# Performance work log

Hardware: AMD Instinct MI355X
Metric: run time of the kernel (lower is better)

## Reference

```python
import jax, jax.numpy as jnp
import numpy as np

EMBED_DIM = 768
NUM_HEADS = 12
HEAD_DIM = EMBED_DIM // NUM_HEADS
SCALE = HEAD_DIM ** -0.5


def setup_inputs() -> dict:
    key = jax.random.key(0)
    k_x, k_wqkv, k_bqkv, k_wfc, k_bfc = jax.random.split(key, 5)
    B, S, D = 32, 577, EMBED_DIM
    x = jax.random.normal(k_x, (B, S, D), dtype=jnp.float32)
    # torch Linear default init ~ U(-1/sqrt(fan_in), 1/sqrt(fan_in)); scale suffices
    lim = 1.0 / np.sqrt(D)
    w_qkv = jax.random.uniform(k_wqkv, (D, 3 * D), jnp.float32, -lim, lim)
    b_qkv = jax.random.uniform(k_bqkv, (3 * D,), jnp.float32, -lim, lim)
    w_fc = jax.random.uniform(k_wfc, (D, D), jnp.float32, -lim, lim)
    b_fc = jax.random.uniform(k_bfc, (D,), jnp.float32, -lim, lim)
    return {"x": x, "w_qkv": w_qkv, "b_qkv": b_qkv, "w_fc": w_fc, "b_fc": b_fc}


def reference(x, w_qkv, b_qkv, w_fc, b_fc):
    B, S, D = x.shape
    H, Dh = NUM_HEADS, HEAD_DIM
    qkv = x @ w_qkv + b_qkv                      # [B,S,3D]
    qkv = qkv.reshape(B, S, 3, H, Dh)
    q, k, v = jnp.moveaxis(qkv, 2, 0)            # each [B,S,H,Dh]
    # scores: [B,H,S,S]
    attn = jnp.einsum('bqhd,bkhd->bhqk', q, k) * SCALE
    attn = jax.nn.softmax(attn, axis=-1)
    out = jnp.einsum('bhqk,bkhd->bqhd', attn, v).reshape(B, S, D)
    # dropout in eval mode -> identity
    return out @ w_fc + b_fc
```

## Files before the change

### kernel.cpp

```cpp
#include <hip/hip_runtime.h>
#include <hip/hip_bf16.h>
#include <stdint.h>

typedef __attribute__((ext_vector_type(8))) short short8;
typedef __attribute__((ext_vector_type(4))) float f32x4;

typedef __attribute__((address_space(3))) uint8_t lds_u8;
typedef __attribute__((address_space(1))) uint8_t glb_u8;

__device__ __forceinline__ void load_lds_16(const void* g, void* l) {
    __builtin_amdgcn_global_load_lds((glb_u8*)g, (lds_u8*)l, 16, 0, 0);
}

__device__ __forceinline__ unsigned short f2b(float f) {
    __hip_bfloat16 h = __float2bfloat16(f);
    return __builtin_bit_cast(unsigned short, h);
}
__device__ __forceinline__ ushort2 f2b2(float a, float b) {
    __hip_bfloat162 h = __float22bfloat162_rn(float2{a, b});
    ushort2 r;
    __builtin_memcpy(&r, &h, sizeof(r));
    return r;
}
__device__ __forceinline__ float b2f(unsigned short u) {
    unsigned int x = ((unsigned int)u) << 16;
    return __builtin_bit_cast(float, x);
}

constexpr int Bz = 32, Ss = 577, Dd = 768, Hh = 12;
constexpr int Mm = Bz * Ss;
constexpr int QKV_N = 3 * Dd;
constexpr float SCALE_L2E = 0.125f * 1.4426950408889634f;

__global__ void cast_f32_bf16(const float* __restrict__ src,
                              unsigned short* __restrict__ dst, int n4) {
    int i = blockIdx.x * blockDim.x + threadIdx.x;
    if (i >= n4) return;
    float4 v = ((const float4*)src)[i];
    ushort4 o;
    o.x = f2b(v.x); o.y = f2b(v.y); o.z = f2b(v.z); o.w = f2b(v.w);
    ((ushort4*)dst)[i] = o;
}

__global__ void transpose_cast(const float* __restrict__ src,
                               unsigned short* __restrict__ dst, int R, int C) {
    __shared__ unsigned short tile[32][33];
    int c0 = blockIdx.x * 32, r0 = blockIdx.y * 32;
    int tx = threadIdx.x, ty = threadIdx.y;
#pragma unroll
    for (int i = 0; i < 4; ++i)
        tile[ty + i * 8][tx] = f2b(src[(size_t)(r0 + ty + i * 8) * C + c0 + tx]);
    __syncthreads();
#pragma unroll
    for (int i = 0; i < 4; ++i) {
        int rr = ty + i * 8;
        dst[(size_t)(c0 + rr) * R + r0 + tx] = tile[tx][rr];
    }
}

template <int N_, bool OUT_BF16>
__global__ __launch_bounds__(512, 2)
void gemm256(const unsigned short* __restrict__ A,
             const unsigned short* __restrict__ Bt,
             const float* __restrict__ bias,
             void* __restrict__ Cout) {
    constexpr int K = 768;
    constexpr int KB = 24;
    constexpr int NX = N_ / 256;
    constexpr int NY = (Mm + 255) / 256;
    constexpr int NWG = NX * NY;
    constexpr int QC = NWG >> 3, RC = NWG & 7;
    extern __shared__ __align__(16) uint8_t smem[];

    const int tid = threadIdx.x;
    const int wave = tid >> 6, lane = tid & 63;
    const int quad = lane >> 4, lc = lane & 15;
    const int wm = wave >> 2, wn = wave & 3;

    const int orig = blockIdx.y * NX + blockIdx.x;
    const int xcd = orig & 7, lid = orig >> 3;
    const int wgid = (xcd < RC ? xcd * (QC + 1) : RC * (QC + 1) + (xcd - RC) * QC) + lid;
    const int tm = (wgid / NX) * 256;
    const int tn = (wgid % NX) * 256;

    const int lrw = wave * 8 + (lane >> 3);
    const unsigned short* apS[2];
    const unsigned short* bpS[2];
#pragma unroll
    for (int s = 0; s < 2; ++s) {
        const int lr = s * 64 + lrw;
        const int chun = (lane & 7) ^ (lr & 7);
        const int trow = lr * 2 + (chun >> 2);
        int ar = tm + trow; if (ar >= Mm) ar = Mm - 1;
        apS[s] = A + (size_t)ar * K + (chun & 3) * 8;
        const int br = tn + trow;
        bpS[s] = Bt + (size_t)br * K + (chun & 3) * 8;
    }

    auto stage = [&](int kb, int buf) {
        uint8_t* d = smem + buf * 32768 + wave * 1024;
        const int ko = kb * 32;
        load_lds_16(apS[0] + ko, d);
        load_lds_16(apS[1] + ko, d + 8192);
        load_lds_16(bpS[0] + ko, d + 16384);
        load_lds_16(bpS[1] + ko, d + 24576);
    };

    const int slotS = (((lane & 1) << 2) + quad) ^ ((lc >> 1) & 7);
    const int aoff = (wm * 64 + (lc >> 1)) * 128 + slotS * 16;
    const int boff = 16384 + (wn * 32 + (lc >> 1)) * 128 + slotS * 16;

    short8 af[8], bf[4];
    auto readfr = [&](int buf) {
        const uint8_t* p = smem + buf * 32768;
#pragma unroll
        for (int m = 0; m < 8; ++m) af[m] = *(const short8*)(p + aoff + m * 1024);
#pragma unroll
        for (int n = 0; n < 4; ++n) bf[n] = *(const short8*)(p + boff + n * 1024);
    };

    f32x4 acc[8][4] = {};
    auto mfmas = [&]() {
        __builtin_amdgcn_s_setprio(1);
#pragma unroll
        for (int m = 0; m < 8; ++m)
#pragma unroll
            for (int n = 0; n < 4; ++n)
                acc[m][n] = __builtin_amdgcn_mfma_f32_16x16x32_bf16(af[m], bf[n], acc[m][n], 0, 0, 0);
        __builtin_amdgcn_s_setprio(0);
    };

    stage(0, 0);
    stage(1, 1);
    asm volatile("s_waitcnt vmcnt(4)" ::: "memory");
    __builtin_amdgcn_s_barrier();

#pragma unroll 1
    for (int t3 = 0; t3 < 7; ++t3) {
        const int T = t3 * 3;
#pragma unroll
        for (int u = 0; u < 3; ++u) {
            const int rb = u;
            const int sb = (u + 2) % 3;
            stage(T + u + 2, sb);
            readfr(rb);
            mfmas();
            asm volatile("s_waitcnt vmcnt(4)" ::: "memory");
            __builtin_amdgcn_s_barrier();
        }
    }
    stage(23, 2);
    readfr(0);
    mfmas();
    asm volatile("s_waitcnt vmcnt(4)" ::: "memory");
    __builtin_amdgcn_s_barrier();
    readfr(1);
    mfmas();
    asm volatile("s_waitcnt vmcnt(0)" ::: "memory");
    __builtin_amdgcn_s_barrier();
    readfr(2);
    mfmas();
    __builtin_amdgcn_s_barrier();

    float bv[4];
#pragma unroll
    for (int j = 0; j < 4; ++j) bv[j] = bias[tn + wn * 64 + j * 16 + lc];

    float* ep = (float*)smem + wave * (16 * 68);
    const int erow = lane >> 2, ec = (lane & 3) * 16;
#pragma unroll
    for (int ia = 0; ia < 8; ++ia) {
#pragma unroll
        for (int j = 0; j < 4; ++j)
#pragma unroll
            for (int r = 0; r < 4; ++r)
                ep[(quad * 4 + r) * 68 + j * 16 + lc] = acc[ia][j][r] + bv[j];
        __threadfence_block();
        int grow = tm + wm * 128 + ia * 16 + erow;
        if (grow < Mm) {
            float4 c0 = *(float4*)&ep[erow * 68 + ec + 0];
            float4 c1 = *(float4*)&ep[erow * 68 + ec + 4];
            float4 c2 = *(float4*)&ep[erow * 68 + ec + 8];
            float4 c3 = *(float4*)&ep[erow * 68 + ec + 12];
            int gcol = tn + wn * 64 + ec;
            if constexpr (OUT_BF16) {
                unsigned short o[16];
                *(ushort2*)&o[0]  = f2b2(c0.x, c0.y);
                *(ushort2*)&o[2]  = f2b2(c0.z, c0.w);
                *(ushort2*)&o[4]  = f2b2(c1.x, c1.y);
                *(ushort2*)&o[6]  = f2b2(c1.z, c1.w);
                *(ushort2*)&o[8]  = f2b2(c2.x, c2.y);
                *(ushort2*)&o[10] = f2b2(c2.z, c2.w);
                *(ushort2*)&o[12] = f2b2(c3.x, c3.y);
                *(ushort2*)&o[14] = f2b2(c3.z, c3.w);
                unsigned short* op = (unsigned short*)Cout + (size_t)grow * N_ + gcol;
                *(short8*)(op + 0) = *(short8*)&o[0];
                *(short8*)(op + 8) = *(short8*)&o[8];
            } else {
                float* op = (float*)Cout + (size_t)grow * N_ + gcol;
                *(float4*)(op + 0)  = c0;
                *(float4*)(op + 4)  = c1;
                *(float4*)(op + 8)  = c2;
                *(float4*)(op + 12) = c3;
            }
        }
        __threadfence_block();
    }
}

__device__ __forceinline__ void attn_tile(
    const unsigned short* __restrict__ Ktile,
    const unsigned short* __restrict__ Vtb,
    unsigned short* __restrict__ Pqw,
    const short8& qf0, const short8& qf1,
    int quad, int lc,
    f32x4 (&oacc)[4], f32x4& lacc) {

    const int sw = lc & 7;
    f32x4 sfr[4];
    __builtin_amdgcn_s_setprio(1);
#pragma unroll
    for (int f = 0; f < 4; ++f) {
        const unsigned short* kr = Ktile + (f * 16 + lc) * 64;
        short8 k0 = *(const short8*)(kr + (quad ^ sw) * 8);
        short8 k1 = *(const short8*)(kr + ((quad ^ 4) ^ sw) * 8);
        f32x4 z = {};
        z = __builtin_amdgcn_mfma_f32_16x16x32_bf16(k0, qf0, z, 0, 0, 0);
        z = __builtin_amdgcn_mfma_f32_16x16x32_bf16(k1, qf1, z, 0, 0, 0);
        sfr[f] = z;
    }
    __builtin_amdgcn_s_setprio(0);

#pragma unroll
    for (int f = 0; f < 4; ++f) {
        float p[4];
#pragma unroll
        for (int r = 0; r < 4; ++r)
            p[r] = __builtin_amdgcn_exp2f(sfr[f][r] * SCALE_L2E);
        ushort2 lo = f2b2(p[0], p[1]), hi = f2b2(p[2], p[3]);
        ushort4 pk = {lo.x, lo.y, hi.x, hi.y};
        *(ushort4*)&Pqw[lc * 72 + f * 16 + quad * 4] = pk;
    }

    __threadfence_block();

    short8 pf0 = *(const short8*)&Pqw[lc * 72 + quad * 8];
    short8 pf1 = *(const short8*)&Pqw[lc * 72 + 32 + quad * 8];
    __builtin_amdgcn_s_setprio(1);
#pragma unroll
    for (int g = 0; g < 4; ++g) {
        short8 vf0 = *(const short8*)&Vtb[(g * 16 + lc) * 80 + quad * 8];
        short8 vf1 = *(const short8*)&Vtb[(g * 16 + lc) * 80 + 32 + quad * 8];
        oacc[g] = __builtin_amdgcn_mfma_f32_16x16x32_bf16(vf0, pf0, oacc[g], 0, 0, 0);
        oacc[g] = __builtin_amdgcn_mfma_f32_16x16x32_bf16(vf1, pf1, oacc[g], 0, 0, 0);
    }
    short8 vo0 = *(const short8*)&Vtb[(64 + lc) * 80 + quad * 8];
    short8 vo1 = *(const short8*)&Vtb[(64 + lc) * 80 + 32 + quad * 8];
    lacc = __builtin_amdgcn_mfma_f32_16x16x32_bf16(vo0, pf0, lacc, 0, 0, 0);
    lacc = __builtin_amdgcn_mfma_f32_16x16x32_bf16(vo1, pf1, lacc, 0, 0, 0);
    __builtin_amdgcn_s_setprio(0);
}

__global__ __launch_bounds__(512)
void attn_kernel(const unsigned short* __restrict__ qkv,
                 unsigned short* __restrict__ outb) {
    __shared__ unsigned short Kt[2][64 * 64];
    __shared__ unsigned short Vt[2][80 * 80];
    __shared__ unsigned short Pq[8][16 * 72];

    const int tid = threadIdx.x;
    const int wave = tid >> 6, lane = tid & 63;
    const int quad = lane >> 4, lc = lane & 15;

    const int orig = (blockIdx.z * gridDim.y + blockIdx.y) * gridDim.x + blockIdx.x;
    const int wgid = (orig & 7) * 240 + (orig >> 3);
    const int qt = wgid % 5;
    const int h  = (wgid / 5) % Hh;
    const int b  = wgid / (5 * Hh);

    const unsigned short* qkvK = qkv + (size_t)b * Ss * QKV_N + h * 64 + 768;
    const unsigned short* qkvV = qkvK + 768;

    const int krow = lane >> 3;
    const int gch = (lane & 7) ^ krow;

    const int qbase = qt * 128 + wave * 16;
    int qrow = qbase + lc; if (qrow > Ss - 1) qrow = Ss - 1;
    const unsigned short* qp = qkv + (size_t)(b * Ss + qrow) * QKV_N + h * 64;
    short8 qf0 = *(const short8*)(qp + quad * 8);
    short8 qf1 = *(const short8*)(qp + 32 + quad * 8);

    unsigned short* Pqw = Pq[wave];

    auto stage_K = [&](int tile, int buf) {
        int key = tile * 64 + wave * 8 + krow;
        const unsigned short* gp = qkvK + (size_t)key * QKV_N + gch * 8;
        load_lds_16(gp, (void*)&Kt[buf][wave * 512]);
    };
    auto load_V = [&](int tile) -> short8 {
        int key = tile * 64 + lane;
        return *(const short8*)(qkvV + (size_t)key * QKV_N + wave * 8);
    };
    auto write_V = [&](short8 v, int buf) {
#pragma unroll
        for (int j = 0; j < 8; ++j)
            Vt[buf][(wave * 8 + j) * 80 + lane] = (unsigned short)v[j];
    };

    if (tid < 80) {
        Vt[0][64 * 80 + tid] = 0x3F80;
        Vt[1][64 * 80 + tid] = 0x3F80;
    }

    f32x4 oacc[4] = {};
    f32x4 lacc = {};

    stage_K(0, 0);
    write_V(load_V(0), 0);
    __syncthreads();

    for (int kb = 0; kb < 8; ++kb) {
        const int buf = kb & 1;
        stage_K(kb + 1, buf ^ 1);
        short8 vreg = load_V(kb + 1);
        attn_tile(Kt[buf], Vt[buf], Pqw, qf0, qf1, quad, lc, oacc, lacc);
        write_V(vreg, buf ^ 1);
        __syncthreads();
    }
    attn_tile(Kt[0], Vt[0], Pqw, qf0, qf1, quad, lc, oacc, lacc);

    float ptail;
    {
        const unsigned short* k576 = qkvK + (size_t)576 * QKV_N;
        short8 kk0 = *(const short8*)(k576 + quad * 8);
        short8 kk1 = *(const short8*)(k576 + 32 + quad * 8);
        float part = 0.f;
#pragma unroll
        for (int j = 0; j < 8; ++j)
            part += b2f((unsigned short)qf0[j]) * b2f((unsigned short)kk0[j])
                  + b2f((unsigned short)qf1[j]) * b2f((unsigned short)kk1[j]);
        part += __shfl_xor(part, 16, 64);
        part += __shfl_xor(part, 32, 64);
        ptail = __builtin_amdgcn_exp2f(part * SCALE_L2E);
        const unsigned short* v576 = qkvV + (size_t)576 * QKV_N;
#pragma unroll
        for (int g = 0; g < 4; ++g) {
            ushort4 vv = *(const ushort4*)(v576 + g * 16 + quad * 4);
            oacc[g][0] += ptail * b2f(vv.x);
            oacc[g][1] += ptail * b2f(vv.y);
            oacc[g][2] += ptail * b2f(vv.z);
            oacc[g][3] += ptail * b2f(vv.w);
        }
    }

    float lq = __shfl(lacc[0], lc, 64) + ptail;
    float inv = 1.f / lq;
#pragma unroll
    for (int g = 0; g < 4; ++g) {
        ushort2 lo = f2b2(oacc[g][0] * inv, oacc[g][1] * inv);
        ushort2 hi = f2b2(oacc[g][2] * inv, oacc[g][3] * inv);
        ushort4 ob = {lo.x, lo.y, hi.x, hi.y};
        *(ushort4*)&Pqw[lc * 72 + g * 16 + quad * 4] = ob;
    }
    __threadfence_block();
#pragma unroll
    for (int p = 0; p < 2; ++p) {
        int lr = p * 8 + (lane >> 3), ch = lane & 7;
        int q = qbase + lr;
        if (q <= Ss - 1) {
            short8 vv = *(const short8*)&Pqw[lr * 72 + ch * 8];
            *(short8*)(outb + (size_t)(b * Ss + q) * Dd + h * 64 + ch * 8) = vv;
        }
    }
}

extern "C" void kernel_launch(void* const* d_in, const int* in_sizes, int n_in,
                              void* d_out, int out_size, void* d_ws, size_t ws_size,
                              hipStream_t stream) {
    const float* x     = (const float*)d_in[0];
    const float* w_qkv = (const float*)d_in[1];
    const float* b_qkv = (const float*)d_in[2];
    const float* w_fc  = (const float*)d_in[3];
    const float* b_fc  = (const float*)d_in[4];

    uint8_t* ws = (uint8_t*)d_ws;
    unsigned short* xb    = (unsigned short*)(ws + 0);
    unsigned short* wqkvT = (unsigned short*)(ws + 28360704);
    unsigned short* wfcT  = (unsigned short*)(ws + 31899648);
    unsigned short* qkv   = (unsigned short*)(ws + 33079296);
    unsigned short* attn  = (unsigned short*)(ws + 118161408);

    static bool lds_init = false;
    if (!lds_init) {
        hipFuncSetAttribute((const void*)gemm256<QKV_N, true>,
                            hipFuncAttributeMaxDynamicSharedMemorySize, 98304);
        hipFuncSetAttribute((const void*)gemm256<Dd, false>,
                            hipFuncAttributeMaxDynamicSharedMemorySize, 98304);
        lds_init = true;
    }

    int n4 = (Mm * Dd) / 4;
    cast_f32_bf16<<<(n4 + 255) / 256, 256, 0, stream>>>(x, xb, n4);
    transpose_cast<<<dim3(QKV_N / 32, Dd / 32), dim3(32, 8), 0, stream>>>(w_qkv, wqkvT, Dd, QKV_N);
    transpose_cast<<<dim3(Dd / 32, Dd / 32), dim3(32, 8), 0, stream>>>(w_fc, wfcT, Dd, Dd);

    gemm256<QKV_N, true><<<dim3(QKV_N / 256, (Mm + 255) / 256), 512, 98304, stream>>>(xb, wqkvT, b_qkv, qkv);

    attn_kernel<<<dim3(5, Hh, Bz), 512, 0, stream>>>(qkv, attn);

    gemm256<Dd, false><<<dim3(Dd / 256, (Mm + 255) / 256), 512, 98304, stream>>>(attn, wfcT, b_fc, d_out);
}
```

Baseline: 312.3 us.

## Give each attention wave 32 query rows to reuse K/V fragments; fuse prep kernels

```diff
diff --git a/kernel.cpp b/kernel.cpp
--- a/kernel.cpp
+++ b/kernel.cpp
@@ -32,21 +32,36 @@
 constexpr int QKV_N = 3 * Dd;
 constexpr float SCALE_L2E = 0.125f * 1.4426950408889634f;
 
-__global__ void cast_f32_bf16(const float* __restrict__ src,
-                              unsigned short* __restrict__ dst, int n4) {
-    int i = blockIdx.x * blockDim.x + threadIdx.x;
-    if (i >= n4) return;
-    float4 v = ((const float4*)src)[i];
-    ushort4 o;
-    o.x = f2b(v.x); o.y = f2b(v.y); o.z = f2b(v.z); o.w = f2b(v.w);
-    ((ushort4*)dst)[i] = o;
-}
-
-__global__ void transpose_cast(const float* __restrict__ src,
-                               unsigned short* __restrict__ dst, int R, int C) {
+__global__ void prep_fused(const float* __restrict__ x, unsigned short* __restrict__ xb,
+                           const float* __restrict__ w_qkv, unsigned short* __restrict__ wqkvT,
+                           const float* __restrict__ w_fc, unsigned short* __restrict__ wfcT) {
+    constexpr int N4 = Mm * Dd / 4;
+    constexpr int NC = N4 / 256;
+    constexpr int NT1 = (QKV_N / 32) * (Dd / 32);
     __shared__ unsigned short tile[32][33];
-    int c0 = blockIdx.x * 32, r0 = blockIdx.y * 32;
-    int tx = threadIdx.x, ty = threadIdx.y;
+
+    const int bid = blockIdx.x;
+    const int tid = threadIdx.x;
+    if (bid < NC) {
+        int i = bid * 256 + tid;
+        float4 v = ((const float4*)x)[i];
+        ushort4 o;
+        o.x = f2b(v.x); o.y = f2b(v.y); o.z = f2b(v.z); o.w = f2b(v.w);
+        ((ushort4*)xb)[i] = o;
+        return;
+    }
+    const float* src; unsigned short* dst; int R, C, bx, by;
+    if (bid < NC + NT1) {
+        int b2 = bid - NC;
+        src = w_qkv; dst = wqkvT; R = Dd; C = QKV_N;
+        bx = b2 % (QKV_N / 32); by = b2 / (QKV_N / 32);
+    } else {
+        int b2 = bid - NC - NT1;
+        src = w_fc; dst = wfcT; R = Dd; C = Dd;
+        bx = b2 % (Dd / 32); by = b2 / (Dd / 32);
+    }
+    int c0 = bx * 32, r0 = by * 32;
+    int tx = tid & 31, ty = tid >> 5;
 #pragma unroll
     for (int i = 0; i < 4; ++i)
         tile[ty + i * 8][tx] = f2b(src[(size_t)(r0 + ty + i * 8) * C + c0 + tx]);
@@ -65,7 +80,6 @@
              const float* __restrict__ bias,
              void* __restrict__ Cout) {
     constexpr int K = 768;
-    constexpr int KB = 24;
     constexpr int NX = N_ / 256;
     constexpr int NY = (Mm + 255) / 256;
     constexpr int NWG = NX * NY;
@@ -140,10 +154,9 @@
         const int T = t3 * 3;
 #pragma unroll
         for (int u = 0; u < 3; ++u) {
-            const int rb = u;
             const int sb = (u + 2) % 3;
             stage(T + u + 2, sb);
-            readfr(rb);
+            readfr(u);
             mfmas();
             asm volatile("s_waitcnt vmcnt(4)" ::: "memory");
             __builtin_amdgcn_s_barrier();
@@ -208,65 +221,12 @@
     }
 }
 
-__device__ __forceinline__ void attn_tile(
-    const unsigned short* __restrict__ Ktile,
-    const unsigned short* __restrict__ Vtb,
-    unsigned short* __restrict__ Pqw,
-    const short8& qf0, const short8& qf1,
-    int quad, int lc,
-    f32x4 (&oacc)[4], f32x4& lacc) {
-
-    const int sw = lc & 7;
-    f32x4 sfr[4];
-    __builtin_amdgcn_s_setprio(1);
-#pragma unroll
-    for (int f = 0; f < 4; ++f) {
-        const unsigned short* kr = Ktile + (f * 16 + lc) * 64;
-        short8 k0 = *(const short8*)(kr + (quad ^ sw) * 8);
-        short8 k1 = *(const short8*)(kr + ((quad ^ 4) ^ sw) * 8);
-        f32x4 z = {};
-        z = __builtin_amdgcn_mfma_f32_16x16x32_bf16(k0, qf0, z, 0, 0, 0);
-        z = __builtin_amdgcn_mfma_f32_16x16x32_bf16(k1, qf1, z, 0, 0, 0);
-        sfr[f] = z;
-    }
-    __builtin_amdgcn_s_setprio(0);
-
-#pragma unroll
-    for (int f = 0; f < 4; ++f) {
-        float p[4];
-#pragma unroll
-        for (int r = 0; r < 4; ++r)
-            p[r] = __builtin_amdgcn_exp2f(sfr[f][r] * SCALE_L2E);
-        ushort2 lo = f2b2(p[0], p[1]), hi = f2b2(p[2], p[3]);
-        ushort4 pk = {lo.x, lo.y, hi.x, hi.y};
-        *(ushort4*)&Pqw[lc * 72 + f * 16 + quad * 4] = pk;
-    }
-
-    __threadfence_block();
-
-    short8 pf0 = *(const short8*)&Pqw[lc * 72 + quad * 8];
-    short8 pf1 = *(const short8*)&Pqw[lc * 72 + 32 + quad * 8];
-    __builtin_amdgcn_s_setprio(1);
-#pragma unroll
-    for (int g = 0; g < 4; ++g) {
-        short8 vf0 = *(const short8*)&Vtb[(g * 16 + lc) * 80 + quad * 8];
-        short8 vf1 = *(const short8*)&Vtb[(g * 16 + lc) * 80 + 32 + quad * 8];
-        oacc[g] = __builtin_amdgcn_mfma_f32_16x16x32_bf16(vf0, pf0, oacc[g], 0, 0, 0);
-        oacc[g] = __builtin_amdgcn_mfma_f32_16x16x32_bf16(vf1, pf1, oacc[g], 0, 0, 0);
-    }
-    short8 vo0 = *(const short8*)&Vtb[(64 + lc) * 80 + quad * 8];
-    short8 vo1 = *(const short8*)&Vtb[(64 + lc) * 80 + 32 + quad * 8];
-    lacc = __builtin_amdgcn_mfma_f32_16x16x32_bf16(vo0, pf0, lacc, 0, 0, 0);
-    lacc = __builtin_amdgcn_mfma_f32_16x16x32_bf16(vo1, pf1, lacc, 0, 0, 0);
-    __builtin_amdgcn_s_setprio(0);
-}
-
-__global__ __launch_bounds__(512)
+__global__ __launch_bounds__(256)
 void attn_kernel(const unsigned short* __restrict__ qkv,
                  unsigned short* __restrict__ outb) {
     __shared__ unsigned short Kt[2][64 * 64];
-    __shared__ unsigned short Vt[2][80 * 80];
-    __shared__ unsigned short Pq[8][16 * 72];
+    __shared__ unsigned short Vt[2][80 * 72];
+    __shared__ unsigned short Pq[4][32 * 72];
 
     const int tid = threadIdx.x;
     const int wave = tid >> 6, lane = tid & 63;
@@ -284,87 +244,165 @@
     const int krow = lane >> 3;
     const int gch = (lane & 7) ^ krow;
 
-    const int qbase = qt * 128 + wave * 16;
-    int qrow = qbase + lc; if (qrow > Ss - 1) qrow = Ss - 1;
-    const unsigned short* qp = qkv + (size_t)(b * Ss + qrow) * QKV_N + h * 64;
-    short8 qf0 = *(const short8*)(qp + quad * 8);
-    short8 qf1 = *(const short8*)(qp + 32 + quad * 8);
+    const int qbase = qt * 128 + wave * 32;
+    short8 qf[2][2];
+#pragma unroll
+    for (int hf = 0; hf < 2; ++hf) {
+        int qrow = qbase + hf * 16 + lc; if (qrow > Ss - 1) qrow = Ss - 1;
+        const unsigned short* qp = qkv + (size_t)(b * Ss + qrow) * QKV_N + h * 64;
+        qf[hf][0] = *(const short8*)(qp + quad * 8);
+        qf[hf][1] = *(const short8*)(qp + 32 + quad * 8);
+    }
 
     unsigned short* Pqw = Pq[wave];
 
     auto stage_K = [&](int tile, int buf) {
-        int key = tile * 64 + wave * 8 + krow;
-        const unsigned short* gp = qkvK + (size_t)key * QKV_N + gch * 8;
-        load_lds_16(gp, (void*)&Kt[buf][wave * 512]);
-    };
-    auto load_V = [&](int tile) -> short8 {
+#pragma unroll
+        for (int s = 0; s < 2; ++s) {
+            int key = tile * 64 + s * 32 + wave * 8 + krow;
+            load_lds_16(qkvK + (size_t)key * QKV_N + gch * 8,
+                        (void*)&Kt[buf][(s * 32 + wave * 8) * 64]);
+        }
+    };
+    auto load_V = [&](int tile, short8 v[2]) {
         int key = tile * 64 + lane;
-        return *(const short8*)(qkvV + (size_t)key * QKV_N + wave * 8);
-    };
-    auto write_V = [&](short8 v, int buf) {
-#pragma unroll
-        for (int j = 0; j < 8; ++j)
-            Vt[buf][(wave * 8 + j) * 80 + lane] = (unsigned short)v[j];
-    };
-
-    if (tid < 80) {
-        Vt[0][64 * 80 + tid] = 0x3F80;
-        Vt[1][64 * 80 + tid] = 0x3F80;
-    }
-
-    f32x4 oacc[4] = {};
-    f32x4 lacc = {};
-
+#pragma unroll
+        for (int s = 0; s < 2; ++s)
+            v[s] = *(const short8*)(qkvV + (size_t)key * QKV_N + (s * 32 + wave * 8));
+    };
+    auto write_V = [&](short8 v[2], int buf) {
+#pragma unroll
+        for (int s = 0; s < 2; ++s)
+#pragma unroll
+            for (int j = 0; j < 8; ++j)
+                Vt[buf][(s * 32 + wave * 8 + j) * 72 + lane] = (unsigned short)v[s][j];
+    };
+
+    if (tid < 72) {
+        Vt[0][64 * 72 + tid] = 0x3F80;
+        Vt[1][64 * 72 + tid] = 0x3F80;
+    }
+
+    f32x4 oacc[2][4] = {};
+    f32x4 lacc[2] = {};
+
+    auto tile_compute = [&](int buf) {
+        const int sw = lc & 7;
+        short8 k0[4], k1[4];
+        #pragma unroll
+        for (int f = 0; f < 4; ++f) {
+            const unsigned short* kr = &Kt[buf][(f * 16 + lc) * 64];
+            k0[f] = *(const short8*)(kr + (quad ^ sw) * 8);
+            k1[f] = *(const short8*)(kr + ((quad ^ 4) ^ sw) * 8);
+        }
+        #pragma unroll
+        for (int hf = 0; hf < 2; ++hf) {
+            f32x4 sfr[4];
+            __builtin_amdgcn_s_setprio(1);
+            #pragma unroll
+            for (int f = 0; f < 4; ++f) {
+                f32x4 z = {};
+                z = __builtin_amdgcn_mfma_f32_16x16x32_bf16(k0[f], qf[hf][0], z, 0, 0, 0);
+                z = __builtin_amdgcn_mfma_f32_16x16x32_bf16(k1[f], qf[hf][1], z, 0, 0, 0);
+                sfr[f] = z;
+            }
+            __builtin_amdgcn_s_setprio(0);
+            #pragma unroll
+            for (int f = 0; f < 4; ++f) {
+                float p0 = __builtin_amdgcn_exp2f(sfr[f][0] * SCALE_L2E);
+                float p1 = __builtin_amdgcn_exp2f(sfr[f][1] * SCALE_L2E);
+                float p2 = __builtin_amdgcn_exp2f(sfr[f][2] * SCALE_L2E);
+                float p3 = __builtin_amdgcn_exp2f(sfr[f][3] * SCALE_L2E);
+                ushort2 lo = f2b2(p0, p1), hi = f2b2(p2, p3);
+                ushort4 pk = {lo.x, lo.y, hi.x, hi.y};
+                *(ushort4*)&Pqw[(hf * 16 + lc) * 72 + f * 16 + quad * 4] = pk;
+            }
+        }
+        __threadfence_block();
+        short8 pf[2][2];
+        #pragma unroll
+        for (int hf = 0; hf < 2; ++hf) {
+            pf[hf][0] = *(const short8*)&Pqw[(hf * 16 + lc) * 72 + quad * 8];
+            pf[hf][1] = *(const short8*)&Pqw[(hf * 16 + lc) * 72 + 32 + quad * 8];
+        }
+        __builtin_amdgcn_s_setprio(1);
+        #pragma unroll
+        for (int g = 0; g < 4; ++g) {
+            short8 vf0 = *(const short8*)&Vt[buf][(g * 16 + lc) * 72 + quad * 8];
+            short8 vf1 = *(const short8*)&Vt[buf][(g * 16 + lc) * 72 + 32 + quad * 8];
+            oacc[0][g] = __builtin_amdgcn_mfma_f32_16x16x32_bf16(vf0, pf[0][0], oacc[0][g], 0, 0, 0);
+            oacc[0][g] = __builtin_amdgcn_mfma_f32_16x16x32_bf16(vf1, pf[0][1], oacc[0][g], 0, 0, 0);
+            oacc[1][g] = __builtin_amdgcn_mfma_f32_16x16x32_bf16(vf0, pf[1][0], oacc[1][g], 0, 0, 0);
+            oacc[1][g] = __builtin_amdgcn_mfma_f32_16x16x32_bf16(vf1, pf[1][1], oacc[1][g], 0, 0, 0);
+        }
+        short8 vo0 = *(const short8*)&Vt[buf][(64 + lc) * 72 + quad * 8];
+        short8 vo1 = *(const short8*)&Vt[buf][(64 + lc) * 72 + 32 + quad * 8];
+        #pragma unroll
+        for (int hf = 0; hf < 2; ++hf) {
+            lacc[hf] = __builtin_amdgcn_mfma_f32_16x16x32_bf16(vo0, pf[hf][0], lacc[hf], 0, 0, 0);
+            lacc[hf] = __builtin_amdgcn_mfma_f32_16x16x32_bf16(vo1, pf[hf][1], lacc[hf], 0, 0, 0);
+        }
+        __builtin_amdgcn_s_setprio(0);
+    };
+
+    short8 vreg[2];
     stage_K(0, 0);
-    write_V(load_V(0), 0);
+    load_V(0, vreg);
+    write_V(vreg, 0);
     __syncthreads();
 
     for (int kb = 0; kb < 8; ++kb) {
         const int buf = kb & 1;
         stage_K(kb + 1, buf ^ 1);
-        short8 vreg = load_V(kb + 1);
-        attn_tile(Kt[buf], Vt[buf], Pqw, qf0, qf1, quad, lc, oacc, lacc);
+        load_V(kb + 1, vreg);
+        tile_compute(buf);
         write_V(vreg, buf ^ 1);
         __syncthreads();
     }
-    attn_tile(Kt[0], Vt[0], Pqw, qf0, qf1, quad, lc, oacc, lacc);
-
-    float ptail;
+    tile_compute(0);
+
+    float ptl[2];
     {
         const unsigned short* k576 = qkvK + (size_t)576 * QKV_N;
         short8 kk0 = *(const short8*)(k576 + quad * 8);
         short8 kk1 = *(const short8*)(k576 + 32 + quad * 8);
-        float part = 0.f;
-#pragma unroll
-        for (int j = 0; j < 8; ++j)
-            part += b2f((unsigned short)qf0[j]) * b2f((unsigned short)kk0[j])
-                  + b2f((unsigned short)qf1[j]) * b2f((unsigned short)kk1[j]);
-        part += __shfl_xor(part, 16, 64);
-        part += __shfl_xor(part, 32, 64);
-        ptail = __builtin_amdgcn_exp2f(part * SCALE_L2E);
         const unsigned short* v576 = qkvV + (size_t)576 * QKV_N;
 #pragma unroll
+        for (int hf = 0; hf < 2; ++hf) {
+            float part = 0.f;
+#pragma unroll
+            for (int j = 0; j < 8; ++j)
+                part += b2f((unsigned short)qf[hf][0][j]) * b2f((unsigned short)kk0[j])
+                      + b2f((unsigned short)qf[hf][1][j]) * b2f((unsigned short)kk1[j]);
+            part += __shfl_xor(part, 16, 64);
+            part += __shfl_xor(part, 32, 64);
+            ptl[hf] = __builtin_amdgcn_exp2f(part * SCALE_L2E);
+#pragma unroll
+            for (int g = 0; g < 4; ++g) {
+                ushort4 vv = *(const ushort4*)(v576 + g * 16 + quad * 4);
+                oacc[hf][g][0] += ptl[hf] * b2f(vv.x);
+                oacc[hf][g][1] += ptl[hf] * b2f(vv.y);
+                oacc[hf][g][2] += ptl[hf] * b2f(vv.z);
+                oacc[hf][g][3] += ptl[hf] * b2f(vv.w);
+            }
+        }
+    }
+
+#pragma unroll
+    for (int hf = 0; hf < 2; ++hf) {
+        float lq = __shfl(lacc[hf][0], lc, 64) + ptl[hf];
+        float inv = 1.f / lq;
+#pragma unroll
         for (int g = 0; g < 4; ++g) {
-            ushort4 vv = *(const ushort4*)(v576 + g * 16 + quad * 4);
-            oacc[g][0] += ptail * b2f(vv.x);
-            oacc[g][1] += ptail * b2f(vv.y);
-            oacc[g][2] += ptail * b2f(vv.z);
-            oacc[g][3] += ptail * b2f(vv.w);
-        }
-    }
-
-    float lq = __shfl(lacc[0], lc, 64) + ptail;
-    float inv = 1.f / lq;
-#pragma unroll
-    for (int g = 0; g < 4; ++g) {
-        ushort2 lo = f2b2(oacc[g][0] * inv, oacc[g][1] * inv);
-        ushort2 hi = f2b2(oacc[g][2] * inv, oacc[g][3] * inv);
-        ushort4 ob = {lo.x, lo.y, hi.x, hi.y};
-        *(ushort4*)&Pqw[lc * 72 + g * 16 + quad * 4] = ob;
+            ushort2 lo = f2b2(oacc[hf][g][0] * inv, oacc[hf][g][1] * inv);
+            ushort2 hi = f2b2(oacc[hf][g][2] * inv, oacc[hf][g][3] * inv);
+            ushort4 ob = {lo.x, lo.y, hi.x, hi.y};
+            *(ushort4*)&Pqw[(hf * 16 + lc) * 72 + g * 16 + quad * 4] = ob;
+        }
     }
     __threadfence_block();
 #pragma unroll
-    for (int p = 0; p < 2; ++p) {
+    for (int p = 0; p < 4; ++p) {
         int lr = p * 8 + (lane >> 3), ch = lane & 7;
         int q = qbase + lr;
         if (q <= Ss - 1) {
@@ -399,14 +437,12 @@
         lds_init = true;
     }
 
-    int n4 = (Mm * Dd) / 4;
-    cast_f32_bf16<<<(n4 + 255) / 256, 256, 0, stream>>>(x, xb, n4);
-    transpose_cast<<<dim3(QKV_N / 32, Dd / 32), dim3(32, 8), 0, stream>>>(w_qkv, wqkvT, Dd, QKV_N);
-    transpose_cast<<<dim3(Dd / 32, Dd / 32), dim3(32, 8), 0, stream>>>(w_fc, wfcT, Dd, Dd);
+    constexpr int PREP_GRID = (Mm * Dd / 4) / 256 + (QKV_N / 32) * (Dd / 32) + (Dd / 32) * (Dd / 32);
+    prep_fused<<<PREP_GRID, 256, 0, stream>>>(x, xb, w_qkv, wqkvT, w_fc, wfcT);
 
     gemm256<QKV_N, true><<<dim3(QKV_N / 256, (Mm + 255) / 256), 512, 98304, stream>>>(xb, wqkvT, b_qkv, qkv);
 
-    attn_kernel<<<dim3(5, Hh, Bz), 512, 0, stream>>>(qkv, attn);
+    attn_kernel<<<dim3(5, Hh, Bz), 256, 0, stream>>>(qkv, attn);
 
     gemm256<Dd, false><<<dim3(Dd / 256, (Mm + 255) / 256), 512, 98304, stream>>>(attn, wfcT, b_fc, d_out);
 }
```

Measured after the change: 307.4 us. Within noise of the previous version (-1.6%).
